# Kernel tuning notes

Hardware: AMD Instinct MI355X
Metric: run time of the kernel (lower is better)

The kernel has to match this reference:

```python
import jax, jax.numpy as jnp
import numpy as np

QUANTSCALE = 0.25
EPS = 1e-5

def act_quant(x):
    # 8-bit symmetric activation quantization, scale per last dim (as in BitNetMCU)
    scale = 127.0 / jnp.maximum(jnp.max(jnp.abs(x), axis=-1, keepdims=True), EPS)
    return jnp.clip(jnp.round(x * scale), -128.0, 127.0) / scale

def wq_binary(w):
    # Binary weights: sign(w - mean) scaled by mean(|w|) (per-tensor)
    scale = jnp.mean(jnp.abs(w))
    return jnp.sign(w - jnp.mean(w)) * scale

def wq_4bitsym(w):
    # 4-bit symmetric levels {+-0.5,...,+-7.5}/scale, per-tensor scale from mean(|w|)
    mag = jnp.maximum(jnp.mean(jnp.abs(w)), EPS)
    scale = QUANTSCALE * 8.0 / mag
    return (jnp.clip(jnp.round(w * scale - 0.5), -8.0, 7.0) + 0.5) / scale

def ste(x, q):
    # straight-through estimator: forward = q, backward = identity
    return x + jax.lax.stop_gradient(q - x)

def rmsnorm(x):
    return x * jax.lax.rsqrt(jnp.mean(x * x, axis=-1, keepdims=True) + EPS)

def bitlinear(x, w):
    xn = rmsnorm(x)                    # NormType='RMS'
    xq = ste(xn, act_quant(xn))
    wq = ste(w, wq_binary(w))          # QuantType='Binary'
    return xq @ wq.T

def bitconv(x, w, groups):
    # NormType='None', QuantType='4bitsym'
    xq = ste(x, act_quant(x))
    wq = ste(w, wq_4bitsym(w))
    return jax.lax.conv_general_dilated(
        xq, wq, window_strides=(1, 1), padding='VALID',
        dimension_numbers=('NCHW', 'OIHW', 'NCHW'),
        feature_group_count=groups)

def setup_inputs() -> dict:
    key = jax.random.key(0)
    ks = jax.random.split(key, 8)
    B, W1, W2, W3 = 16384, 512, 512, 512
    return {
        'x':        jax.random.normal(ks[0], (B, 1, 16, 16), jnp.float32),
        'conv1_w':  jax.random.normal(ks[1], (16, 1, 3, 3), jnp.float32) * 0.1,
        'conv1b_w': jax.random.normal(ks[2], (16, 1, 3, 3), jnp.float32) * 0.1,
        'conv2_w':  jax.random.normal(ks[3], (96, 1, 12, 12), jnp.float32) * 0.1,
        'fc1_w':    jax.random.normal(ks[4], (W1, 96), jnp.float32) * 0.1,
        'fc2_w':    jax.random.normal(ks[5], (W2, W1), jnp.float32) * 0.1,
        'fc3_w':    jax.random.normal(ks[6], (W3, W2), jnp.float32) * 0.1,
        'fcl_w':    jax.random.normal(ks[7], (10, W3), jnp.float32) * 0.1,
    }

def reference(x, conv1_w, conv1b_w, conv2_w, fc1_w, fc2_w, fc3_w, fcl_w):
    h = jax.nn.relu(bitconv(x, conv1_w, 1))    # [B,16,14,14]
    h = jax.nn.relu(bitconv(h, conv1b_w, 16))  # depthwise -> [B,16,12,12]
    h = jax.nn.relu(bitconv(h, conv2_w, 16))   # grouped k12 -> [B,96,1,1]
    h = h.reshape(h.shape[0], -1)              # [B,96]
    h = jax.nn.relu(bitlinear(h, fc1_w))
    h = jax.nn.relu(bitlinear(h, fc2_w))
    h = jax.nn.relu(bitlinear(h, fc3_w))
    return bitlinear(h, fcl_w)                 # [B,10] logits (dropout is eval no-op)
```

## Files before the change

kernel.cpp:

```cpp
#include <hip/hip_runtime.h>
#include <math.h>

#define EPSQ 1e-5

typedef int v4i  __attribute__((ext_vector_type(4)));
typedef int v16i __attribute__((ext_vector_type(16)));

__device__ void bstat(const float* __restrict__ w, int cnt, double2* dst, int divn) {
    __shared__ double ls[4], la[4];
    int t = threadIdx.x;
    double s = 0.0, a = 0.0;
    const float4* w4 = (const float4*)w;
    int nv = cnt >> 2;
    for (int i = t; i < nv; i += 256) {
        float4 v = w4[i];
        s += (double)v.x + (double)v.y + (double)v.z + (double)v.w;
        a += fabs((double)v.x) + fabs((double)v.y) + fabs((double)v.z) + fabs((double)v.w);
    }
    for (int o = 32; o; o >>= 1) { s += __shfl_down(s, o); a += __shfl_down(a, o); }
    if ((t & 63) == 0) { ls[t >> 6] = s; la[t >> 6] = a; }
    __syncthreads();
    if (t == 0) {
        for (int i = 1; i < 4; i++) { s += ls[i]; a += la[i]; }
        if (divn > 0) { dst->x = s / divn; dst->y = a / divn; }
        else          { dst->x = s;        dst->y = a; }
    }
}

__global__ __launch_bounds__(256) void wstats_part(
    const float* __restrict__ a0, const float* __restrict__ a1,
    const float* __restrict__ a2, const float* __restrict__ a3,
    const float* __restrict__ a4, const float* __restrict__ a5,
    const float* __restrict__ a6, double2* __restrict__ part,
    double2* __restrict__ stats) {
    int b = blockIdx.x;
    if      (b == 0) bstat(a0, 144,   stats + 0, 144);
    else if (b == 1) bstat(a1, 144,   stats + 1, 144);
    else if (b == 2) bstat(a2, 13824, stats + 2, 13824);
    else if (b == 3) bstat(a6, 5120,  stats + 6, 5120);
    else if (b < 8)  bstat(a3 + (b - 4)  * 12288, 12288, part + (b - 4), 0);
    else if (b < 24) bstat(a4 + (b - 8)  * 16384, 16384, part + 4 + (b - 8), 0);
    else             bstat(a5 + (b - 24) * 16384, 16384, part + 20 + (b - 24), 0);
}

__global__ __launch_bounds__(64) void wstats_comb(const double2* __restrict__ part,
                                                  double2* __restrict__ stats) {
    int t = threadIdx.x;
    if (t == 0) {
        double s = 0, a = 0;
        for (int i = 0; i < 4; i++) { s += part[i].x; a += part[i].y; }
        stats[3].x = s / 49152.0; stats[3].y = a / 49152.0;
    } else if (t == 1) {
        double s = 0, a = 0;
        for (int i = 4; i < 20; i++) { s += part[i].x; a += part[i].y; }
        stats[4].x = s / 262144.0; stats[4].y = a / 262144.0;
    } else if (t == 2) {
        double s = 0, a = 0;
        for (int i = 20; i < 36; i++) { s += part[i].x; a += part[i].y; }
        stats[5].x = s / 262144.0; stats[5].y = a / 262144.0;
    }
}

__device__ inline float q4odd(float w, double mag) {
    double sc = 2.0 / fmax(mag, EPSQ);
    double q = fmin(fmax(rint((double)w * sc - 0.5), -8.0), 7.0);
    return (float)(2.0 * q + 1.0);
}

__global__ __launch_bounds__(256) void wq_conv(
    const float* __restrict__ wc1, const float* __restrict__ wc1b,
    const float* __restrict__ wc2, const double2* __restrict__ stats,
    float* __restrict__ c1o, float* __restrict__ c1bo, float* __restrict__ c2o) {
    int i = blockIdx.x * 256 + threadIdx.x;
    if (i < 144) c1o[i] = q4odd(wc1[i], stats[0].y);
    else if (i < 288) c1bo[i - 144] = q4odd(wc1b[i - 144], stats[1].y);
    else if (i < 288 + 13824) { int j = i - 288; c2o[j] = q4odd(wc2[j], stats[2].y); }
}

__device__ inline char bsign(float w, double mean) {
    double d = (double)w - mean;
    return d > 0.0 ? (char)1 : (d < 0.0 ? (char)-1 : (char)0);
}

__global__ __launch_bounds__(256) void wq_fc(
    const float* __restrict__ wfc1, const float* __restrict__ wfc2,
    const float* __restrict__ wfc3, const float* __restrict__ wfcl,
    const double2* __restrict__ stats,
    char* __restrict__ f1, char* __restrict__ f2,
    char* __restrict__ f3, char* __restrict__ fl) {
    int i = blockIdx.x * 256 + threadIdx.x;
    if (i < 65536) {
        int row = i >> 7, k = i & 127;
        f1[i] = (k < 96) ? bsign(wfc1[row * 96 + k], stats[3].x) : (char)0;
        return;
    }
    i -= 65536;
    if (i < 262144) { f2[i] = bsign(wfc2[i], stats[4].x); return; }
    i -= 262144;
    if (i < 262144) { f3[i] = bsign(wfc3[i], stats[5].x); return; }
    i -= 262144;
    if (i < 5120)   { fl[i] = bsign(wfcl[i], stats[6].x); }
}

template <int Wd>
__device__ inline double cpix(const float (&rq)[3][Wd], const float* wv,
                              const double* inv, int qx) {
    float d0 = rq[0][qx] * wv[0] + rq[0][qx + 1] * wv[1] + rq[0][qx + 2] * wv[2];
    float d1 = rq[1][qx] * wv[3] + rq[1][qx + 1] * wv[4] + rq[1][qx + 2] * wv[5];
    float d2 = rq[2][qx] * wv[6] + rq[2][qx + 1] * wv[7] + rq[2][qx + 2] * wv[8];
    return (double)d0 * inv[0] + (double)d1 * inv[1] + (double)d2 * inv[2];
}

__global__ __launch_bounds__(256) void conv_fused(
    const float* __restrict__ x, const float* __restrict__ w1o,
    const float* __restrict__ w1bo, const float* __restrict__ w2o,
    const double2* __restrict__ stats,
    char* __restrict__ xq96, double* __restrict__ arow) {
    __shared__ float sxp[16][17];
    __shared__ double sinv0[16];
    __shared__ float sh1[16][14][15];
    __shared__ double sinv1[16][14];
    __shared__ float sh2[16][12][13];
    __shared__ double sinv2[16][12];
    __shared__ float sw1[144], sw1b[144];
    __shared__ double sh3p[2][96];
    __shared__ double sh3[96];
    __shared__ double srs[2];
    int b = blockIdx.x, t = threadIdx.x;
    double cw1  = fmax(stats[0].y, EPSQ) * 0.25;
    double cw1b = fmax(stats[1].y, EPSQ) * 0.25;
    double cw2  = fmax(stats[2].y, EPSQ) * 0.25;

    float v = x[(size_t)b * 256 + t];
    if (t < 144) { sw1[t] = w1o[t]; sw1b[t] = w1bo[t]; }
    float m = fabsf(v);
    for (int o = 8; o; o >>= 1) m = fmaxf(m, __shfl_xor(m, o));
    double s0 = 127.0 / fmax((double)m, EPSQ);
    sxp[t >> 4][t & 15] = (float)rint((double)v * s0);
    if ((t & 15) == 0) sinv0[t >> 4] = 1.0 / s0;
    __syncthreads();

    if (t < 224) {
        int c = t / 14, r = t % 14;
        float rq[3][16]; double inv[3];
        #pragma unroll
        for (int i = 0; i < 3; i++) {
            inv[i] = sinv0[r + i] * cw1;
            #pragma unroll
            for (int j = 0; j < 16; j++) rq[i][j] = sxp[r + i][j];
        }
        float wv[9];
        #pragma unroll
        for (int k = 0; k < 9; k++) wv[k] = sw1[c * 9 + k];
        double vals[14]; double mx = 0.0;
        #pragma unroll
        for (int qx = 0; qx < 14; qx++) {
            vals[qx] = fmax(cpix(rq, wv, inv, qx), 0.0);
            mx = fmax(mx, vals[qx]);
        }
        double s2 = 127.0 / fmax(mx, EPSQ);
        sinv1[c][r] = 1.0 / s2;
        #pragma unroll
        for (int qx = 0; qx < 14; qx++)
            sh1[c][r][qx] = (float)rint(vals[qx] * s2);
    }
    __syncthreads();

    if (t < 192) {
        int c = t / 12, r = t % 12;
        float rq[3][14]; double inv[3];
        #pragma unroll
        for (int i = 0; i < 3; i++) {
            inv[i] = sinv1[c][r + i] * cw1b;
            #pragma unroll
            for (int j = 0; j < 14; j++) rq[i][j] = sh1[c][r + i][j];
        }
        float wv[9];
        #pragma unroll
        for (int k = 0; k < 9; k++) wv[k] = sw1b[c * 9 + k];
        double vals[12]; double mx = 0.0;
        #pragma unroll
        for (int qx = 0; qx < 12; qx++) {
            vals[qx] = fmax(cpix(rq, wv, inv, qx), 0.0);
            mx = fmax(mx, vals[qx]);
        }
        double s3 = 127.0 / fmax(mx, EPSQ);
        sinv2[c][r] = 1.0 / s3;
        #pragma unroll
        for (int qx = 0; qx < 12; qx++)
            sh2[c][r][qx] = (float)rint(vals[qx] * s3);
    }
    __syncthreads();

    if (t < 192) {
        int o = t % 96, half = t / 96;
        int g = o / 6;
        const float* wk = w2o + o * 144 + half * 72;
        double acc = 0.0;
        #pragma unroll
        for (int hh = 0; hh < 6; hh++) {
            int row = half * 6 + hh;
            float4 w0 = *(const float4*)(wk + hh * 12);
            float4 w1 = *(const float4*)(wk + hh * 12 + 4);
            float4 w2v = *(const float4*)(wk + hh * 12 + 8);
            const float* sr = &sh2[g][row][0];
            float d = 0.f;
            d += sr[0] * w0.x; d += sr[1] * w0.y; d += sr[2] * w0.z; d += sr[3] * w0.w;
            d += sr[4] * w1.x; d += sr[5] * w1.y; d += sr[6] * w1.z; d += sr[7] * w1.w;
            d += sr[8] * w2v.x; d += sr[9] * w2v.y; d += sr[10] * w2v.z; d += sr[11] * w2v.w;
            acc += (double)d * sinv2[g][row];
        }
        sh3p[half][o] = acc;
    }
    __syncthreads();
    if (t < 96) sh3[t] = fmax((sh3p[0][t] + sh3p[1][t]) * cw2, 0.0);
    __syncthreads();

    if (t < 64) {
        double a = sh3[t];
        double bb = (t < 32) ? sh3[64 + t] : 0.0;
        double ss = a * a + bb * bb;
        double mxx = fmax(fabs(a), fabs(bb));
        for (int o = 32; o; o >>= 1) {
            ss += __shfl_down(ss, o);
            mxx = fmax(mxx, __shfl_down(mxx, o));
        }
        if (t == 0) {
            double r = 1.0 / sqrt(ss / 96.0 + 1e-5);
            double s4 = 127.0 / fmax(mxx * r, EPSQ);
            srs[0] = r; srs[1] = s4;
        }
    }
    __syncthreads();
    if (t < 128) {
        char q = 0;
        if (t < 96) {
            double xn = sh3[t] * srs[0];
            q = (char)(int)rint(xn * srs[1]);
        }
        xq96[(size_t)b * 128 + t] = q;
        if (t == 0) arow[b] = 1.0 / srs[1];
    }
}

__global__ __launch_bounds__(256, 2) void fc_fused(
    const char* __restrict__ Xq, const char* __restrict__ Wq, int K,
    const double2* __restrict__ stats, int sidx,
    double* __restrict__ arow, char* __restrict__ xq) {
    __shared__ char As[32 * 128];
    __shared__ char Bs[512 * 128];
    __shared__ double redS[4][32];
    __shared__ int    redM[4][32];
    __shared__ double csrow[32];
    int t = threadIdx.x;
    int lane = t & 63;
    int w = t >> 6;
    int m0 = blockIdx.x * 32;

    v16i acc[4] = {};

    for (int k0 = 0; k0 < K; k0 += 128) {
        {
            int row = t >> 3, cb = (t & 7) * 16;
            *(int4*)(As + row * 128 + (cb ^ ((row & 7) << 4))) =
                *(const int4*)(Xq + (size_t)(m0 + row) * K + k0 + cb);
        }
        #pragma unroll
        for (int p = 0; p < 16; p++) {
            int slot = p * 256 + t;
            int row = slot >> 3, cb = (slot & 7) * 16;
            *(int4*)(Bs + row * 128 + (cb ^ ((row & 7) << 4))) =
                *(const int4*)(Wq + (size_t)row * K + k0 + cb);
        }
        __syncthreads();
        int ra = lane & 31;
        int ksel = (lane >> 5) * 16;
        #pragma unroll
        for (int kk = 0; kk < 4; kk++) {
            int kb = kk * 32 + ksel;
            v4i a = *(v4i*)(As + ra * 128 + (kb ^ ((ra & 7) << 4)));
            #pragma unroll
            for (int nt = 0; nt < 4; nt++) {
                int rb = w * 128 + nt * 32 + (lane & 31);
                v4i bb = *(v4i*)(Bs + rb * 128 + (kb ^ ((rb & 7) << 4)));
                acc[nt] = __builtin_amdgcn_mfma_i32_32x32x32_i8(a, bb, acc[nt], 0, 0, 0);
            }
        }
        __syncthreads();
    }

    double ps[16]; int pm[16];
    #pragma unroll
    for (int reg = 0; reg < 16; reg++) {
        int v0 = max(acc[0][reg], 0), v1 = max(acc[1][reg], 0);
        int v2 = max(acc[2][reg], 0), v3 = max(acc[3][reg], 0);
        acc[0][reg] = v0; acc[1][reg] = v1; acc[2][reg] = v2; acc[3][reg] = v3;
        ps[reg] = (double)v0 * v0 + (double)v1 * v1 + (double)v2 * v2 + (double)v3 * v3;
        pm[reg] = max(max(v0, v1), max(v2, v3));
    }
    #pragma unroll
    for (int o = 1; o < 32; o <<= 1) {
        #pragma unroll
        for (int reg = 0; reg < 16; reg++) {
            ps[reg] += __shfl_xor(ps[reg], o);
            pm[reg] = max(pm[reg], __shfl_xor(pm[reg], o));
        }
    }
    if ((lane & 31) == 0) {
        int h = lane >> 5;
        #pragma unroll
        for (int reg = 0; reg < 16; reg++) {
            int row = (reg & 3) + 8 * (reg >> 2) + 4 * h;
            redS[w][row] = ps[reg];
            redM[w][row] = pm[reg];
        }
    }
    __syncthreads();
    if (t < 32) {
        double S = redS[0][t] + redS[1][t] + redS[2][t] + redS[3][t];
        int M = max(max(redM[0][t], redM[1][t]), max(redM[2][t], redM[3][t]));
        double c = stats[sidx].y * arow[m0 + t];
        double mean = S * c * c / 512.0;
        double r = 1.0 / sqrt(mean + 1e-5);
        double s = 127.0 / fmax((double)M * c * r, EPSQ);
        csrow[t] = c * r * s;
        arow[m0 + t] = 1.0 / s;
    }
    __syncthreads();

    #pragma unroll
    for (int nt = 0; nt < 4; nt++) {
        int col = w * 128 + nt * 32 + (lane & 31);
        #pragma unroll
        for (int reg = 0; reg < 16; reg++) {
            int row = (reg & 3) + 8 * (reg >> 2) + 4 * (lane >> 5);
            Bs[row * 512 + col] = (char)(int)rint((double)acc[nt][reg] * csrow[row]);
        }
    }
    __syncthreads();
    #pragma unroll
    for (int i = 0; i < 4; i++) {
        int idx = i * 256 + t;
        *(int4*)(xq + (size_t)m0 * 512 + idx * 16) = *(const int4*)(Bs + idx * 16);
    }
}

__device__ inline int bdot(int a, int b) {
    int r = ((a << 24) >> 24) * ((b << 24) >> 24);
    r += ((a << 16) >> 24) * ((b << 16) >> 24);
    r += ((a << 8) >> 24) * ((b << 8) >> 24);
    r += (a >> 24) * (b >> 24);
    return r;
}

__global__ __launch_bounds__(256) void fcl_k(const char* __restrict__ Xq,
                                             const char* __restrict__ Wq,
                                             const double* __restrict__ arow,
                                             const double2* __restrict__ stats,
                                             float* __restrict__ out) {
    int gi = blockIdx.x * 256 + threadIdx.x;
    int mrow = gi / 10, n = gi - mrow * 10;
    const int4* xp = (const int4*)(Xq + (size_t)mrow * 512);
    const int4* wp = (const int4*)(Wq + n * 512);
    int acc = 0;
    #pragma unroll 8
    for (int i = 0; i < 32; i++) {
        int4 a = xp[i], b = wp[i];
        acc += bdot(a.x, b.x) + bdot(a.y, b.y) + bdot(a.z, b.z) + bdot(a.w, b.w);
    }
    out[gi] = (float)((double)acc * stats[6].y * arow[mrow]);
}

extern "C" void kernel_launch(void* const* d_in, const int* in_sizes, int n_in,
                              void* d_out, int out_size, void* d_ws, size_t ws_size,
                              hipStream_t stream) {
    const float* x     = (const float*)d_in[0];
    const float* w_c1  = (const float*)d_in[1];
    const float* w_c1b = (const float*)d_in[2];
    const float* w_c2  = (const float*)d_in[3];
    const float* w_fc1 = (const float*)d_in[4];
    const float* w_fc2 = (const float*)d_in[5];
    const float* w_fc3 = (const float*)d_in[6];
    const float* w_fcl = (const float*)d_in[7];
    float* out = (float*)d_out;
    char* wsb = (char*)d_ws;
    const int B = 16384;

    float*   c1o   = (float*)(wsb + 0);
    float*   c1bo  = (float*)(wsb + 1024);
    float*   c2o   = (float*)(wsb + 2048);
    double2* stats = (double2*)(wsb + 57344);
    double2* part  = (double2*)(wsb + 57856);
    char*    f1q   = wsb + 65536;
    char*    f2q   = wsb + 131072;
    char*    f3q   = wsb + 393216;
    char*    flq   = wsb + 655360;
    double*  arow  = (double*)(wsb + 663552);
    char*    xq96  = wsb + 1048576;
    char*    xq512 = wsb + 3145728;

    wstats_part<<<40, 256, 0, stream>>>(w_c1, w_c1b, w_c2, w_fc1, w_fc2, w_fc3,
                                        w_fcl, part, stats);
    wstats_comb<<<1, 64, 0, stream>>>(part, stats);
    wq_conv<<<56, 256, 0, stream>>>(w_c1, w_c1b, w_c2, stats, c1o, c1bo, c2o);
    wq_fc<<<2324, 256, 0, stream>>>(w_fc1, w_fc2, w_fc3, w_fcl, stats, f1q, f2q, f3q, flq);

    conv_fused<<<B, 256, 0, stream>>>(x, c1o, c1bo, c2o, stats, xq96, arow);

    fc_fused<<<B / 32, 256, 0, stream>>>(xq96,  f1q, 128, stats, 3, arow, xq512);
    fc_fused<<<B / 32, 256, 0, stream>>>(xq512, f2q, 512, stats, 4, arow, xq512);
    fc_fused<<<B / 32, 256, 0, stream>>>(xq512, f3q, 512, stats, 5, arow, xq512);

    fcl_k<<<640, 256, 0, stream>>>(xq512, flq, arow, stats, out);
}
```

Measured before the change: 247.3 us.

## Pack conv activations as int8 and double the FC row tile to 64

In the conv stage, the quantized intermediate activations are stored in shared memory as packed bytes instead of floats. The conv2 weights are precomputed as int8, so the grouped 12x12 convolution becomes an integer byte dot product. The input tile is padded so it can be read with float4 loads. In the FC layers, each block now covers 64 rows instead of 32, reusing each loaded weight tile across two MFMA row tiles. That halves the grid to 256 blocks and doubles the accumulator registers, which may reduce occupancy and latency hiding.

```diff
diff --git a/kernel.cpp b/kernel.cpp
--- a/kernel.cpp
+++ b/kernel.cpp
@@ -70,11 +70,14 @@
 __global__ __launch_bounds__(256) void wq_conv(
     const float* __restrict__ wc1, const float* __restrict__ wc1b,
     const float* __restrict__ wc2, const double2* __restrict__ stats,
-    float* __restrict__ c1o, float* __restrict__ c1bo, float* __restrict__ c2o) {
+    float* __restrict__ c1o, float* __restrict__ c1bo, char* __restrict__ c2i) {
     int i = blockIdx.x * 256 + threadIdx.x;
     if (i < 144) c1o[i] = q4odd(wc1[i], stats[0].y);
     else if (i < 288) c1bo[i - 144] = q4odd(wc1b[i - 144], stats[1].y);
-    else if (i < 288 + 13824) { int j = i - 288; c2o[j] = q4odd(wc2[j], stats[2].y); }
+    else if (i < 288 + 13824) {
+        int j = i - 288;
+        c2i[j] = (char)(int)q4odd(wc2[j], stats[2].y);
+    }
 }
 
 __device__ inline char bsign(float w, double mean) {
@@ -102,6 +105,14 @@
     if (i < 5120)   { fl[i] = bsign(wfcl[i], stats[6].x); }
 }
 
+__device__ inline int bdot(int a, int b) {
+    int r = ((a << 24) >> 24) * ((b << 24) >> 24);
+    r += ((a << 16) >> 24) * ((b << 16) >> 24);
+    r += ((a << 8) >> 24) * ((b << 8) >> 24);
+    r += (a >> 24) * (b >> 24);
+    return r;
+}
+
 template <int Wd>
 __device__ inline double cpix(const float (&rq)[3][Wd], const float* wv,
                               const double* inv, int qx) {
@@ -113,14 +124,14 @@
 
 __global__ __launch_bounds__(256) void conv_fused(
     const float* __restrict__ x, const float* __restrict__ w1o,
-    const float* __restrict__ w1bo, const float* __restrict__ w2o,
+    const float* __restrict__ w1bo, const char* __restrict__ w2i,
     const double2* __restrict__ stats,
     char* __restrict__ xq96, double* __restrict__ arow) {
-    __shared__ float sxp[16][17];
+    __shared__ float sxp[16][20];
     __shared__ double sinv0[16];
-    __shared__ float sh1[16][14][15];
+    __shared__ unsigned int sh1[16][14][5];
     __shared__ double sinv1[16][14];
-    __shared__ float sh2[16][12][13];
+    __shared__ unsigned int sh2[16][12][3];
     __shared__ double sinv2[16][12];
     __shared__ float sw1[144], sw1b[144];
     __shared__ double sh3p[2][96];
@@ -147,7 +158,8 @@
         for (int i = 0; i < 3; i++) {
             inv[i] = sinv0[r + i] * cw1;
             #pragma unroll
-            for (int j = 0; j < 16; j++) rq[i][j] = sxp[r + i][j];
+            for (int q4 = 0; q4 < 4; q4++)
+                *(float4*)&rq[i][q4 * 4] = *(const float4*)&sxp[r + i][q4 * 4];
         }
         float wv[9];
         #pragma unroll
@@ -160,9 +172,14 @@
         }
         double s2 = 127.0 / fmax(mx, EPSQ);
         sinv1[c][r] = 1.0 / s2;
-        #pragma unroll
-        for (int qx = 0; qx < 14; qx++)
-            sh1[c][r][qx] = (float)rint(vals[qx] * s2);
+        unsigned int pk[4] = {0u, 0u, 0u, 0u};
+        #pragma unroll
+        for (int qx = 0; qx < 14; qx++) {
+            unsigned int q = (unsigned int)(int)rint(vals[qx] * s2);
+            pk[qx >> 2] |= q << ((qx & 3) * 8);
+        }
+        #pragma unroll
+        for (int j = 0; j < 4; j++) sh1[c][r][j] = pk[j];
     }
     __syncthreads();
 
@@ -172,8 +189,13 @@
         #pragma unroll
         for (int i = 0; i < 3; i++) {
             inv[i] = sinv1[c][r + i] * cw1b;
-            #pragma unroll
-            for (int j = 0; j < 14; j++) rq[i][j] = sh1[c][r + i][j];
+            unsigned int w0 = sh1[c][r + i][0], w1 = sh1[c][r + i][1];
+            unsigned int w2d = sh1[c][r + i][2], w3 = sh1[c][r + i][3];
+            #pragma unroll
+            for (int j = 0; j < 14; j++) {
+                unsigned int wd = (j < 4) ? w0 : (j < 8) ? w1 : (j < 12) ? w2d : w3;
+                rq[i][j] = (float)((wd >> ((j & 3) * 8)) & 0xffu);
+            }
         }
         float wv[9];
         #pragma unroll
@@ -186,28 +208,29 @@
         }
         double s3 = 127.0 / fmax(mx, EPSQ);
         sinv2[c][r] = 1.0 / s3;
-        #pragma unroll
-        for (int qx = 0; qx < 12; qx++)
-            sh2[c][r][qx] = (float)rint(vals[qx] * s3);
+        unsigned int pk[3] = {0u, 0u, 0u};
+        #pragma unroll
+        for (int qx = 0; qx < 12; qx++) {
+            unsigned int q = (unsigned int)(int)rint(vals[qx] * s3);
+            pk[qx >> 2] |= q << ((qx & 3) * 8);
+        }
+        #pragma unroll
+        for (int j = 0; j < 3; j++) sh2[c][r][j] = pk[j];
     }
     __syncthreads();
 
     if (t < 192) {
         int o = t % 96, half = t / 96;
         int g = o / 6;
-        const float* wk = w2o + o * 144 + half * 72;
+        const int* wk = (const int*)(w2i + o * 144 + half * 72);
         double acc = 0.0;
         #pragma unroll
         for (int hh = 0; hh < 6; hh++) {
             int row = half * 6 + hh;
-            float4 w0 = *(const float4*)(wk + hh * 12);
-            float4 w1 = *(const float4*)(wk + hh * 12 + 4);
-            float4 w2v = *(const float4*)(wk + hh * 12 + 8);
-            const float* sr = &sh2[g][row][0];
-            float d = 0.f;
-            d += sr[0] * w0.x; d += sr[1] * w0.y; d += sr[2] * w0.z; d += sr[3] * w0.w;
-            d += sr[4] * w1.x; d += sr[5] * w1.y; d += sr[6] * w1.z; d += sr[7] * w1.w;
-            d += sr[8] * w2v.x; d += sr[9] * w2v.y; d += sr[10] * w2v.z; d += sr[11] * w2v.w;
+            int d = 0;
+            #pragma unroll
+            for (int j = 0; j < 3; j++)
+                d += bdot((int)sh2[g][row][j], wk[hh * 3 + j]);
             acc += (double)d * sinv2[g][row];
         }
         sh3p[half][o] = acc;
@@ -247,21 +270,23 @@
     const char* __restrict__ Xq, const char* __restrict__ Wq, int K,
     const double2* __restrict__ stats, int sidx,
     double* __restrict__ arow, char* __restrict__ xq) {
-    __shared__ char As[32 * 128];
+    __shared__ char As[64 * 128];
     __shared__ char Bs[512 * 128];
-    __shared__ double redS[4][32];
-    __shared__ int    redM[4][32];
-    __shared__ double csrow[32];
+    __shared__ double redS[4][64];
+    __shared__ int    redM[4][64];
+    __shared__ double csrow[64];
     int t = threadIdx.x;
     int lane = t & 63;
     int w = t >> 6;
-    int m0 = blockIdx.x * 32;
-
-    v16i acc[4] = {};
+    int m0 = blockIdx.x * 64;
+
+    v16i acc[2][4] = {};
 
     for (int k0 = 0; k0 < K; k0 += 128) {
-        {
-            int row = t >> 3, cb = (t & 7) * 16;
+        #pragma unroll
+        for (int p = 0; p < 2; p++) {
+            int slot = p * 256 + t;
+            int row = slot >> 3, cb = (slot & 7) * 16;
             *(int4*)(As + row * 128 + (cb ^ ((row & 7) << 4))) =
                 *(const int4*)(Xq + (size_t)(m0 + row) * K + k0 + cb);
         }
@@ -273,50 +298,55 @@
                 *(const int4*)(Wq + (size_t)row * K + k0 + cb);
         }
         __syncthreads();
-        int ra = lane & 31;
         int ksel = (lane >> 5) * 16;
+        int ra0 = lane & 31, ra1 = 32 + (lane & 31);
         #pragma unroll
         for (int kk = 0; kk < 4; kk++) {
             int kb = kk * 32 + ksel;
-            v4i a = *(v4i*)(As + ra * 128 + (kb ^ ((ra & 7) << 4)));
+            v4i a0 = *(v4i*)(As + ra0 * 128 + (kb ^ ((ra0 & 7) << 4)));
+            v4i a1 = *(v4i*)(As + ra1 * 128 + (kb ^ ((ra1 & 7) << 4)));
             #pragma unroll
             for (int nt = 0; nt < 4; nt++) {
                 int rb = w * 128 + nt * 32 + (lane & 31);
                 v4i bb = *(v4i*)(Bs + rb * 128 + (kb ^ ((rb & 7) << 4)));
-                acc[nt] = __builtin_amdgcn_mfma_i32_32x32x32_i8(a, bb, acc[nt], 0, 0, 0);
+                acc[0][nt] = __builtin_amdgcn_mfma_i32_32x32x32_i8(a0, bb, acc[0][nt], 0, 0, 0);
+                acc[1][nt] = __builtin_amdgcn_mfma_i32_32x32x32_i8(a1, bb, acc[1][nt], 0, 0, 0);
             }
         }
         __syncthreads();
     }
 
-    double ps[16]; int pm[16];
     #pragma unroll
-    for (int reg = 0; reg < 16; reg++) {
-        int v0 = max(acc[0][reg], 0), v1 = max(acc[1][reg], 0);
-        int v2 = max(acc[2][reg], 0), v3 = max(acc[3][reg], 0);
-        acc[0][reg] = v0; acc[1][reg] = v1; acc[2][reg] = v2; acc[3][reg] = v3;
-        ps[reg] = (double)v0 * v0 + (double)v1 * v1 + (double)v2 * v2 + (double)v3 * v3;
-        pm[reg] = max(max(v0, v1), max(v2, v3));
-    }
-    #pragma unroll
-    for (int o = 1; o < 32; o <<= 1) {
+    for (int mt = 0; mt < 2; mt++) {
+        double ps[16]; int pm[16];
         #pragma unroll
         for (int reg = 0; reg < 16; reg++) {
-            ps[reg] += __shfl_xor(ps[reg], o);
-            pm[reg] = max(pm[reg], __shfl_xor(pm[reg], o));
-        }
-    }
-    if ((lane & 31) == 0) {
-        int h = lane >> 5;
-        #pragma unroll
-        for (int reg = 0; reg < 16; reg++) {
-            int row = (reg & 3) + 8 * (reg >> 2) + 4 * h;
-            redS[w][row] = ps[reg];
-            redM[w][row] = pm[reg];
-        }
-    }
-    __syncthreads();
-    if (t < 32) {
+            int v0 = max(acc[mt][0][reg], 0), v1 = max(acc[mt][1][reg], 0);
+            int v2 = max(acc[mt][2][reg], 0), v3 = max(acc[mt][3][reg], 0);
+            acc[mt][0][reg] = v0; acc[mt][1][reg] = v1;
+            acc[mt][2][reg] = v2; acc[mt][3][reg] = v3;
+            ps[reg] = (double)v0 * v0 + (double)v1 * v1 + (double)v2 * v2 + (double)v3 * v3;
+            pm[reg] = max(max(v0, v1), max(v2, v3));
+        }
+        #pragma unroll
+        for (int o = 1; o < 32; o <<= 1)
+            #pragma unroll
+            for (int reg = 0; reg < 16; reg++) {
+                ps[reg] += __shfl_xor(ps[reg], o);
+                pm[reg] = max(pm[reg], __shfl_xor(pm[reg], o));
+            }
+        if ((lane & 31) == 0) {
+            int h = lane >> 5;
+            #pragma unroll
+            for (int reg = 0; reg < 16; reg++) {
+                int row = mt * 32 + (reg & 3) + 8 * (reg >> 2) + 4 * h;
+                redS[w][row] = ps[reg];
+                redM[w][row] = pm[reg];
+            }
+        }
+    }
+    __syncthreads();
+    if (t < 64) {
         double S = redS[0][t] + redS[1][t] + redS[2][t] + redS[3][t];
         int M = max(max(redM[0][t], redM[1][t]), max(redM[2][t], redM[3][t]));
         double c = stats[sidx].y * arow[m0 + t];
@@ -329,28 +359,22 @@
     __syncthreads();
 
     #pragma unroll
-    for (int nt = 0; nt < 4; nt++) {
-        int col = w * 128 + nt * 32 + (lane & 31);
-        #pragma unroll
-        for (int reg = 0; reg < 16; reg++) {
-            int row = (reg & 3) + 8 * (reg >> 2) + 4 * (lane >> 5);
-            Bs[row * 512 + col] = (char)(int)rint((double)acc[nt][reg] * csrow[row]);
-        }
-    }
+    for (int mt = 0; mt < 2; mt++)
+        #pragma unroll
+        for (int nt = 0; nt < 4; nt++) {
+            int col = w * 128 + nt * 32 + (lane & 31);
+            #pragma unroll
+            for (int reg = 0; reg < 16; reg++) {
+                int row = mt * 32 + (reg & 3) + 8 * (reg >> 2) + 4 * (lane >> 5);
+                Bs[row * 512 + col] = (char)(int)rint((double)acc[mt][nt][reg] * csrow[row]);
+            }
+        }
     __syncthreads();
     #pragma unroll
-    for (int i = 0; i < 4; i++) {
+    for (int i = 0; i < 8; i++) {
         int idx = i * 256 + t;
         *(int4*)(xq + (size_t)m0 * 512 + idx * 16) = *(const int4*)(Bs + idx * 16);
     }
-}
-
-__device__ inline int bdot(int a, int b) {
-    int r = ((a << 24) >> 24) * ((b << 24) >> 24);
-    r += ((a << 16) >> 24) * ((b << 16) >> 24);
-    r += ((a << 8) >> 24) * ((b << 8) >> 24);
-    r += (a >> 24) * (b >> 24);
-    return r;
 }
 
 __global__ __launch_bounds__(256) void fcl_k(const char* __restrict__ Xq,
@@ -388,7 +412,7 @@
 
     float*   c1o   = (float*)(wsb + 0);
     float*   c1bo  = (float*)(wsb + 1024);
-    float*   c2o   = (float*)(wsb + 2048);
+    char*    c2i   = wsb + 2048;
     double2* stats = (double2*)(wsb + 57344);
     double2* part  = (double2*)(wsb + 57856);
     char*    f1q   = wsb + 65536;
@@ -402,14 +426,14 @@
     wstats_part<<<40, 256, 0, stream>>>(w_c1, w_c1b, w_c2, w_fc1, w_fc2, w_fc3,
                                         w_fcl, part, stats);
     wstats_comb<<<1, 64, 0, stream>>>(part, stats);
-    wq_conv<<<56, 256, 0, stream>>>(w_c1, w_c1b, w_c2, stats, c1o, c1bo, c2o);
+    wq_conv<<<56, 256, 0, stream>>>(w_c1, w_c1b, w_c2, stats, c1o, c1bo, c2i);
     wq_fc<<<2324, 256, 0, stream>>>(w_fc1, w_fc2, w_fc3, w_fcl, stats, f1q, f2q, f3q, flq);
 
-    conv_fused<<<B, 256, 0, stream>>>(x, c1o, c1bo, c2o, stats, xq96, arow);
-
-    fc_fused<<<B / 32, 256, 0, stream>>>(xq96,  f1q, 128, stats, 3, arow, xq512);
-    fc_fused<<<B / 32, 256, 0, stream>>>(xq512, f2q, 512, stats, 4, arow, xq512);
-    fc_fused<<<B / 32, 256, 0, stream>>>(xq512, f3q, 512, stats, 5, arow, xq512);
+    conv_fused<<<B, 256, 0, stream>>>(x, c1o, c1bo, c2i, stats, xq96, arow);
+
+    fc_fused<<<B / 64, 256, 0, stream>>>(xq96,  f1q, 128, stats, 3, arow, xq512);
+    fc_fused<<<B / 64, 256, 0, stream>>>(xq512, f2q, 512, stats, 4, arow, xq512);
+    fc_fused<<<B / 64, 256, 0, stream>>>(xq512, f3q, 512, stats, 5, arow, xq512);
 
     fcl_k<<<640, 256, 0, stream>>>(xq512, flq, arow, stats, out);
 }
```

After: 340.5 us. 37.7% more time.
